# Kernel optimization log

Hardware: AMD Instinct MI355X
Metric: run time of the kernel (lower is better)

The kernel has to match this reference:

```python
import jax, jax.numpy as jnp
import numpy as np

N_NODES = 100_000
N_EDGES = 1_600_000
F_IN = 32
F_OUT = 32
DIM = 2
K = 5                      # kernel_size per dim (open spline)
KTOT = K ** DIM            # 25 kernel weight matrices
S = 2 ** DIM               # 4 nonzero linear-B-spline basis terms per edge
NEG_SLOPE = 0.2

# offsets over the 2^DIM corners of the spline cell, [S, DIM]
_OFFSETS = np.array([[(s >> d) & 1 for d in range(DIM)] for s in range(S)], dtype=np.int32)
_STRIDES = np.array([K ** d for d in range(DIM)], dtype=np.int32)


def _spline_basis(pseudo):
    """Degree-1 open B-spline basis. pseudo: [E, DIM] in [0,1].
    Returns basis [E, S] and kernel-weight indices widx [E, S]."""
    offsets = jnp.asarray(_OFFSETS)
    strides = jnp.asarray(_STRIDES)
    p = pseudo * (K - 1)                         # open spline scaling
    fl = jnp.floor(p)
    frac = p - fl                                # [E, DIM]
    b = jnp.where(offsets[None] == 0, 1.0 - frac[:, None, :], frac[:, None, :])
    basis = jnp.prod(b, axis=-1)                 # [E, S]
    idx = jnp.clip(fl.astype(jnp.int32)[:, None, :] + offsets[None], 0, K - 1)
    widx = jnp.sum(idx * strides, axis=-1)       # [E, S] in [0, KTOT)
    return basis, widx


def setup_inputs() -> dict:
    key = jax.random.key(0)
    ks = jax.random.split(key, 7)
    x = jax.random.normal(ks[0], (N_NODES, F_IN), dtype=jnp.float32)
    edge_index = jax.random.randint(ks[1], (2, N_EDGES), 0, N_NODES)
    pseudo = jax.random.uniform(ks[2], (N_EDGES, DIM), dtype=jnp.float32)
    bound = 1.0 / np.sqrt(KTOT * F_IN)           # matches reset_parameters uniform(size, ...)
    weight = jax.random.uniform(ks[3], (KTOT, F_IN, F_OUT), jnp.float32, -bound, bound)
    root_weight = jax.random.uniform(ks[4], (F_IN, F_OUT), jnp.float32, -bound, bound)
    att_weight = jax.random.uniform(ks[5], (2 * F_OUT,), jnp.float32, -bound, bound)
    bias = jax.random.uniform(ks[6], (F_OUT,), jnp.float32, -bound, bound)
    return {"x": x, "edge_index": edge_index, "pseudo": pseudo, "weight": weight,
            "root_weight": root_weight, "att_weight": att_weight, "bias": bias}


def reference(x, edge_index, pseudo, weight, root_weight, att_weight, bias):
    row, col = edge_index[0], edge_index[1]      # row = target, col = source
    basis, widx = _spline_basis(pseudo)          # [E,S], [E,S]

    # Precompute x @ W_k for every kernel weight: [N, KTOT, F_OUT]
    xw = jnp.einsum('nf,kfo->nko', x, weight)
    flat = col[:, None] * KTOT + widx            # [E, S] flat (node, kernel) index
    gathered = xw.reshape(-1, F_OUT)[flat]       # [E, S, F_OUT]
    msg = jnp.einsum('es,esf->ef', basis, gathered)  # spline-weighted edge messages

    x_root = x @ root_weight                     # [N, F_OUT]

    # GAT-style attention logits: cat([x_root[row], msg]) . att_weight
    alpha = x_root[row] @ att_weight[:F_OUT] + msg @ att_weight[F_OUT:]
    alpha = jnp.where(alpha > 0, alpha, NEG_SLOPE * alpha)  # leaky relu

    # segment softmax over incoming edges of each target node
    amax = jax.ops.segment_max(alpha, row, num_segments=N_NODES)
    amax = jnp.where(jnp.isfinite(amax), amax, 0.0)
    ex = jnp.exp(alpha - amax[row])
    denom = jax.ops.segment_sum(ex, row, num_segments=N_NODES)
    att = ex / (denom[row] + 1e-16)

    out = jax.ops.segment_sum(msg * att[:, None], row, num_segments=N_NODES)
    return out + x_root + bias
```

## Files before the change

kernel.cpp:

```cpp
#include <hip/hip_runtime.h>
#include <stdint.h>

#define N_NODES 100000
#define N_EDGES 1600000
#define NBLK_SCAN 391

typedef __attribute__((ext_vector_type(8))) short short8;
typedef __attribute__((ext_vector_type(4))) float float4v;

__device__ __forceinline__ unsigned short f32_to_bf16(float f) {
  uint32_t u = __float_as_uint(f);
  u += 0x7fffu + ((u >> 16) & 1u);
  return (unsigned short)(u >> 16);
}
__device__ __forceinline__ float bf16_to_f32(unsigned short h) {
  return __uint_as_float(((uint32_t)h) << 16);
}

__global__ __launch_bounds__(256) void k_zero(
    const float* __restrict__ weight, const float* __restrict__ root_w,
    const float* __restrict__ att_w,
    int* __restrict__ deg, unsigned short* __restrict__ wbf,
    unsigned short* __restrict__ xw) {
  int tid = threadIdx.x;
  int b = blockIdx.x;
  int i = b * 256 + tid;
  if (i < N_NODES) deg[i] = 0;
  if (b < 100) {
    int e = i;
    int t = e >> 9, rem = e & 511;
    int q = rem >> 7, row = (rem >> 3) & 15, j = rem & 7;
    int km = t >> 1, fin = q * 8 + j, fo = (t & 1) * 16 + row;
    wbf[e] = f32_to_bf16(weight[(km * 32 + fin) * 32 + fo]);
  } else if (b == 100) {
    for (int idx = tid; idx < 1024; idx += 256) {
      int t = 50 + (idx >> 9), rem = idx & 511;
      int q = rem >> 7, row = (rem >> 3) & 15, j = rem & 7;
      int fin = q * 8 + j, fo = (t - 50) * 16 + row;
      wbf[t * 512 + rem] = f32_to_bf16(root_w[fin * 32 + fo]);
    }
    for (int idx = tid; idx < 1024; idx += 256) {
      int t = 52 + (idx >> 9), rem = idx & 511;
      int q = rem >> 7, row = (rem >> 3) & 15, j = rem & 7;
      int fin = q * 8 + j, km = (t - 52) * 16 + row;
      float s = 0.f;
      if (km < 25) {
#pragma unroll
        for (int fo = 0; fo < 32; fo++)
          s += weight[(km * 32 + fin) * 32 + fo] * att_w[32 + fo];
      }
      wbf[t * 512 + rem] = f32_to_bf16(s);
    }
  } else if (b == 101) {
    if (tid < 400) ((unsigned int*)(xw + 80000000))[tid] = 0u;
  }
}

__global__ __launch_bounds__(256) void k1_xw(
    const float* __restrict__ x, const unsigned short* __restrict__ wbf,
    const int* __restrict__ ei, const float* __restrict__ att_w,
    const float* __restrict__ bias,
    int* __restrict__ deg, unsigned short* __restrict__ rank,
    unsigned short* __restrict__ xw, float* __restrict__ out,
    uint2* __restrict__ od, float* __restrict__ ydot) {
  __shared__ __align__(16) uint2 st[3200];
  int tid = threadIdx.x;
  int b = blockIdx.x;

  int e = b * 256 + tid;
  int rk = atomicAdd(&deg[ei[e]], 1);

  int wave = tid >> 6, lane = tid & 63;
  int quad = lane >> 4, c16 = lane & 15;
  int n0 = b * 16;
  int node = n0 + c16;
  const float* xp = x + (size_t)node * 32 + quad * 8;
  float4 a0 = *reinterpret_cast<const float4*>(xp);
  float4 a1 = *reinterpret_cast<const float4*>(xp + 4);
  short8 af;
  af[0] = (short)f32_to_bf16(a0.x); af[1] = (short)f32_to_bf16(a0.y);
  af[2] = (short)f32_to_bf16(a0.z); af[3] = (short)f32_to_bf16(a0.w);
  af[4] = (short)f32_to_bf16(a1.x); af[5] = (short)f32_to_bf16(a1.y);
  af[6] = (short)f32_to_bf16(a1.z); af[7] = (short)f32_to_bf16(a1.w);

  float rsum = 0.f;
#pragma unroll 1
  for (int idx = 0; idx < 13; idx++) {
    int t = wave * 13 + idx;
    short8 bf = *reinterpret_cast<const short8*>(wbf + ((t * 4 + quad) * 16 + c16) * 8);
    float4v acc = {0.f, 0.f, 0.f, 0.f};
    acc = __builtin_amdgcn_mfma_f32_16x16x32_bf16(bf, af, acc, 0, 0, 0);
    if (t < 50) {
      uint2 pk;
      pk.x = (unsigned int)f32_to_bf16(acc[0]) |
             ((unsigned int)f32_to_bf16(acc[1]) << 16);
      pk.y = (unsigned int)f32_to_bf16(acc[2]) |
             ((unsigned int)f32_to_bf16(acc[3]) << 16);
      int tq = t * 4 + quad;
      st[tq * 16 + (c16 ^ (tq & 15))] = pk;
    } else {
      int gfo = (t - 50) * 16 + quad * 4;
      float4 bi = *reinterpret_cast<const float4*>(bias + gfo);
      float4 o;
      o.x = acc[0] + bi.x; o.y = acc[1] + bi.y;
      o.z = acc[2] + bi.z; o.w = acc[3] + bi.w;
      *reinterpret_cast<float4*>(out + (size_t)node * 32 + gfo) = o;
      float4 aw = *reinterpret_cast<const float4*>(att_w + gfo);
      rsum += acc[0] * aw.x + acc[1] * aw.y + acc[2] * aw.z + acc[3] * aw.w;
    }
  }
  if (wave < 2) {
    int t = 52 + wave;
    short8 bf = *reinterpret_cast<const short8*>(wbf + ((t * 4 + quad) * 16 + c16) * 8);
    float4v acc = {0.f, 0.f, 0.f, 0.f};
    acc = __builtin_amdgcn_mfma_f32_16x16x32_bf16(bf, af, acc, 0, 0, 0);
    float4 o;
    o.x = acc[0]; o.y = acc[1]; o.z = acc[2]; o.w = acc[3];
    *reinterpret_cast<float4*>(ydot + (size_t)node * 32 + (t - 52) * 16 + quad * 4) = o;
  }
  if (wave == 3) {
    rsum += __shfl_xor(rsum, 16);
    rsum += __shfl_xor(rsum, 32);
    if (lane < 16) od[node].y = __float_as_uint(rsum);
  }
  __syncthreads();
  uint2* dst = reinterpret_cast<uint2*>(xw) + (size_t)n0 * 200;
  for (int j = tid; j < 3200; j += 256) {
    int nd = j / 200;
    int tq = j - nd * 200;
    dst[j] = st[tq * 16 + (nd ^ (tq & 15))];
  }
  rank[e] = (unsigned short)rk;
}

__global__ __launch_bounds__(256) void kscan1(const int* __restrict__ deg,
                                              int* __restrict__ incl,
                                              int* __restrict__ bsum) {
  __shared__ int s[256];
  int tid = threadIdx.x;
  int i = blockIdx.x * 256 + tid;
  int v = (i < N_NODES) ? deg[i] : 0;
  s[tid] = v;
  __syncthreads();
  for (int d = 1; d < 256; d <<= 1) {
    int t = (tid >= d) ? s[tid - d] : 0;
    __syncthreads();
    s[tid] += t;
    __syncthreads();
  }
  if (i < N_NODES) incl[i] = s[tid];
  if (tid == 255) bsum[blockIdx.x] = s[255];
}

__global__ __launch_bounds__(512) void kscan2(const int* __restrict__ bsum,
                                              int* __restrict__ bbase) {
  __shared__ int s[512];
  int tid = threadIdx.x;
  int v = (tid < NBLK_SCAN) ? bsum[tid] : 0;
  s[tid] = v;
  __syncthreads();
  for (int d = 1; d < 512; d <<= 1) {
    int t = (tid >= d) ? s[tid - d] : 0;
    __syncthreads();
    s[tid] += t;
    __syncthreads();
  }
  if (tid < NBLK_SCAN) bbase[tid] = s[tid] - v;
}

__global__ __launch_bounds__(256) void kscan3(const int* __restrict__ deg,
                                              int* __restrict__ offs,
                                              const int* __restrict__ bbase,
                                              uint2* __restrict__ od) {
  int i = blockIdx.x * 256 + threadIdx.x;
  if (i < N_NODES) {
    int v = offs[i] - deg[i] + bbase[i >> 8];
    offs[i] = v;
    od[i].x = (unsigned int)v;
  }
  if (i == 0) offs[N_NODES] = N_EDGES;
}

__global__ __launch_bounds__(256) void k_ydq(const float* __restrict__ ydot,
                                             uint2* __restrict__ ydq) {
  int idx = blockIdx.x * 256 + threadIdx.x;
  int n = idx >> 4, cell = idx & 15;
  int i1 = cell >> 2, i0 = cell & 3;
  const float* bb = ydot + (size_t)n * 32 + i1 * 5 + i0;
  float y0 = bb[0], y1 = bb[1], y2 = bb[5], y3 = bb[6];
  uint2 pk;
  pk.x = (unsigned int)f32_to_bf16(y0) | ((unsigned int)f32_to_bf16(y1) << 16);
  pk.y = (unsigned int)f32_to_bf16(y2) | ((unsigned int)f32_to_bf16(y3) << 16);
  ydq[idx] = pk;
}

__global__ __launch_bounds__(256) void kscatter(
    const int* __restrict__ ei, const float* __restrict__ pseudo,
    const uint2* __restrict__ od, const unsigned short* __restrict__ rank,
    const uint2* __restrict__ ydq,
    unsigned int* __restrict__ eidx, uint2* __restrict__ ecoef) {
  int e = blockIdx.x * 256 + threadIdx.x;
  int r = ei[e];
  int c = ei[N_EDGES + e];
  float p0 = pseudo[2 * e] * 4.f;
  float p1 = pseudo[2 * e + 1] * 4.f;
  int rk = rank[e];
  uint2 v = od[r];
  float fl0 = floorf(p0), fl1 = floorf(p1);
  float fr0 = p0 - fl0, fr1 = p1 - fl1;
  int i0 = (int)fl0, i1 = (int)fl1;
  uint2 yq = ydq[c * 16 + i1 * 4 + i0];
  float y0 = __uint_as_float(yq.x << 16);
  float y1 = __uint_as_float(yq.x & 0xffff0000u);
  float y2 = __uint_as_float(yq.y << 16);
  float y3 = __uint_as_float(yq.y & 0xffff0000u);
  float c0 = 1.f - fr0, c1 = 1.f - fr1;
  float b0 = c0 * c1, b1 = fr0 * c1, b2 = c0 * fr1, b3 = fr0 * fr1;
  float alpha = __uint_as_float(v.y) + b0 * y0 + b1 * y1 + b2 * y2 + b3 * y3;
  alpha = alpha > 0.f ? alpha : 0.2f * alpha;
  float ex = __expf(alpha);
  int pos = (int)v.x + rk;
  int w0 = i0 + 5 * i1;
  int w2 = w0 + 5;
  uint2 pk;
  pk.x = (unsigned int)f32_to_bf16(b0 * ex) |
         ((unsigned int)f32_to_bf16(b1 * ex) << 16);
  pk.y = (unsigned int)f32_to_bf16(b2 * ex) |
         ((unsigned int)f32_to_bf16(b3 * ex) << 16);
  ecoef[pos] = pk;
  eidx[pos] = (unsigned int)c | ((unsigned int)w0 << 17) |
              ((unsigned int)w2 << 22);
}

__global__ __launch_bounds__(256) void k2_csr(
    const int* __restrict__ offs, const unsigned int* __restrict__ eidx,
    const uint2* __restrict__ ecoef, const unsigned short* __restrict__ xw,
    float* __restrict__ out) {
  int tid = threadIdx.x;
  int wave = tid >> 6, lane = tid & 63;
  int node = blockIdx.x * 4 + wave;
  if (node >= N_NODES) return;
  int f = lane & 31, half = lane >> 5;
  int s0 = offs[node], s1 = offs[node + 1];
  const unsigned short* xwf = xw + f;
  float accA = 0.f, accB = 0.f, denA = 0.f, denB = 0.f;
  int i = s0 + half;

  for (; i + 6 < s1; i += 8) {
    unsigned int id[4];
    uint2 cf[4];
    id[0] = eidx[i];     id[1] = eidx[i + 2];
    id[2] = eidx[i + 4]; id[3] = eidx[i + 6];
    cf[0] = ecoef[i];     cf[1] = ecoef[i + 2];
    cf[2] = ecoef[i + 4]; cf[3] = ecoef[i + 6];
    float g0[4], g1[4], g2[4], g3[4];
#pragma unroll
    for (int u = 0; u < 4; u++) {
      const unsigned short* base = xwf + (size_t)(id[u] & 0x1FFFF) * 800;
      int o0 = ((id[u] >> 17) & 31) * 32;
      int o2 = ((id[u] >> 22) & 31) * 32;
      g0[u] = bf16_to_f32(base[o0]);
      g1[u] = bf16_to_f32(base[o0 + 32]);
      g2[u] = bf16_to_f32(base[o2]);
      g3[u] = bf16_to_f32(base[o2 + 32]);
    }
#pragma unroll
    for (int u = 0; u < 4; u++) {
      float q0 = __uint_as_float(cf[u].x << 16);
      float q1 = __uint_as_float(cf[u].x & 0xffff0000u);
      float q2 = __uint_as_float(cf[u].y << 16);
      float q3 = __uint_as_float(cf[u].y & 0xffff0000u);
      float m = q0 * g0[u] + q1 * g1[u] + q2 * g2[u] + q3 * g3[u];
      float d = (q0 + q1) + (q2 + q3);
      if (u & 1) { accB += m; denB += d; } else { accA += m; denA += d; }
    }
  }
  for (; i < s1; i += 2) {
    unsigned int idv = eidx[i];
    uint2 cfv = ecoef[i];
    const unsigned short* base = xwf + (size_t)(idv & 0x1FFFF) * 800;
    int o0 = ((idv >> 17) & 31) * 32;
    int o2 = ((idv >> 22) & 31) * 32;
    float g0 = bf16_to_f32(base[o0]);
    float g1 = bf16_to_f32(base[o0 + 32]);
    float g2 = bf16_to_f32(base[o2]);
    float g3 = bf16_to_f32(base[o2 + 32]);
    float q0 = __uint_as_float(cfv.x << 16);
    float q1 = __uint_as_float(cfv.x & 0xffff0000u);
    float q2 = __uint_as_float(cfv.y << 16);
    float q3 = __uint_as_float(cfv.y & 0xffff0000u);
    accA += q0 * g0 + q1 * g1 + q2 * g2 + q3 * g3;
    denA += (q0 + q1) + (q2 + q3);
  }

  float acc = accA + accB;
  float den = denA + denB;
  acc += __shfl_xor(acc, 32);
  den += __shfl_xor(den, 32);
  if (half == 0) out[node * 32 + f] += acc / (den + 1e-16f);
}

extern "C" void kernel_launch(void* const* d_in, const int* in_sizes, int n_in,
                              void* d_out, int out_size, void* d_ws, size_t ws_size,
                              hipStream_t stream) {
  const float* x      = (const float*)d_in[0];
  const int*   ei     = (const int*)d_in[1];
  const float* pseudo = (const float*)d_in[2];
  const float* weight = (const float*)d_in[3];
  const float* root_w = (const float*)d_in[4];
  const float* att_w  = (const float*)d_in[5];
  const float* bias   = (const float*)d_in[6];
  float* out = (float*)d_out;

  char* ws = (char*)d_ws;
  unsigned short* xw   = (unsigned short*)ws;
  uint2* ydq           = (uint2*)(ws + 160001600);
  uint2* od            = (uint2*)(ws + 172801600);
  unsigned short* wbf  = (unsigned short*)(ws + 173601600);
  int* deg             = (int*)(ws + 173656896);
  int* offs            = (int*)(ws + 174056896);
  int* bsum            = (int*)(ws + 174456912);
  int* bbase           = (int*)(ws + 174458512);
  unsigned short* rank = (unsigned short*)(ws + 174460112);
  uint2* ecoef         = (uint2*)(ws + 177660112);
  float* ydot          = (float*)(ws + 177660112);
  unsigned int* eidx   = (unsigned int*)(ws + 190460112);

  hipLaunchKernelGGL(k_zero, dim3(NBLK_SCAN), dim3(256), 0, stream,
                     weight, root_w, att_w, deg, wbf, xw);
  hipLaunchKernelGGL(k1_xw, dim3(6250), dim3(256), 0, stream,
                     x, wbf, ei, att_w, bias, deg, rank, xw, out, od, ydot);
  hipLaunchKernelGGL(kscan1, dim3(NBLK_SCAN), dim3(256), 0, stream, deg, offs, bsum);
  hipLaunchKernelGGL(kscan2, dim3(1), dim3(512), 0, stream, bsum, bbase);
  hipLaunchKernelGGL(kscan3, dim3(NBLK_SCAN), dim3(256), 0, stream, deg, offs, bbase, od);
  hipLaunchKernelGGL(k_ydq, dim3(6250), dim3(256), 0, stream, ydot, ydq);
  hipLaunchKernelGGL(kscatter, dim3(6250), dim3(256), 0, stream,
                     ei, pseudo, od, rank, ydq, eidx, ecoef);
  hipLaunchKernelGGL(k2_csr, dim3(25000), dim3(256), 0, stream,
                     offs, eidx, ecoef, xw, out);
}
```

Measured before the change: 382.7 us.

## Fuse ydq packing into xw kernel and split degree histogram into its own kernel

The per-node attention-dot cell packing (ydq) is now computed inside the xw MFMA kernel from a shared-memory staging tile. This removes the separate k_ydq kernel and the fp32 ydot round trip through global memory. The edge degree atomic histogram moves out of the xw kernel into its own kernel, which decouples the atomic latency from the MFMA work but adds a launch and reads edge_index in a separate pass. The main loop's unroll-1 pragma is also dropped, letting the compiler unroll it.

```diff
diff --git a/kernel.cpp b/kernel.cpp
--- a/kernel.cpp
+++ b/kernel.cpp
@@ -56,19 +56,23 @@
   }
 }
 
-__global__ __launch_bounds__(256) void k1_xw(
+__global__ __launch_bounds__(256) void k1a_hist(
+    const int* __restrict__ ei, int* __restrict__ deg,
+    unsigned short* __restrict__ rank) {
+  int e = blockIdx.x * 256 + threadIdx.x;
+  int r = ei[e];
+  rank[e] = (unsigned short)atomicAdd(&deg[r], 1);
+}
+
+__global__ __launch_bounds__(256) void k1b_xw(
     const float* __restrict__ x, const unsigned short* __restrict__ wbf,
-    const int* __restrict__ ei, const float* __restrict__ att_w,
-    const float* __restrict__ bias,
-    int* __restrict__ deg, unsigned short* __restrict__ rank,
+    const float* __restrict__ att_w, const float* __restrict__ bias,
     unsigned short* __restrict__ xw, float* __restrict__ out,
-    uint2* __restrict__ od, float* __restrict__ ydot) {
+    uint2* __restrict__ od, uint2* __restrict__ ydq) {
   __shared__ __align__(16) uint2 st[3200];
+  __shared__ float ydl[16][33];
   int tid = threadIdx.x;
   int b = blockIdx.x;
-
-  int e = b * 256 + tid;
-  int rk = atomicAdd(&deg[ei[e]], 1);
 
   int wave = tid >> 6, lane = tid & 63;
   int quad = lane >> 4, c16 = lane & 15;
@@ -84,7 +88,6 @@
   af[6] = (short)f32_to_bf16(a1.z); af[7] = (short)f32_to_bf16(a1.w);
 
   float rsum = 0.f;
-#pragma unroll 1
   for (int idx = 0; idx < 13; idx++) {
     int t = wave * 13 + idx;
     short8 bf = *reinterpret_cast<const short8*>(wbf + ((t * 4 + quad) * 16 + c16) * 8);
@@ -114,9 +117,9 @@
     short8 bf = *reinterpret_cast<const short8*>(wbf + ((t * 4 + quad) * 16 + c16) * 8);
     float4v acc = {0.f, 0.f, 0.f, 0.f};
     acc = __builtin_amdgcn_mfma_f32_16x16x32_bf16(bf, af, acc, 0, 0, 0);
-    float4 o;
-    o.x = acc[0]; o.y = acc[1]; o.z = acc[2]; o.w = acc[3];
-    *reinterpret_cast<float4*>(ydot + (size_t)node * 32 + (t - 52) * 16 + quad * 4) = o;
+    int kmb = wave * 16 + quad * 4;
+#pragma unroll
+    for (int r2 = 0; r2 < 4; r2++) ydl[c16][kmb + r2] = acc[r2];
   }
   if (wave == 3) {
     rsum += __shfl_xor(rsum, 16);
@@ -124,13 +127,23 @@
     if (lane < 16) od[node].y = __float_as_uint(rsum);
   }
   __syncthreads();
+  {
+    int nd = tid >> 4, cell = tid & 15;
+    int i1c = cell >> 2, i0c = cell & 3;
+    int km0 = i1c * 5 + i0c;
+    float y0 = ydl[nd][km0], y1 = ydl[nd][km0 + 1];
+    float y2 = ydl[nd][km0 + 5], y3 = ydl[nd][km0 + 6];
+    uint2 pk;
+    pk.x = (unsigned int)f32_to_bf16(y0) | ((unsigned int)f32_to_bf16(y1) << 16);
+    pk.y = (unsigned int)f32_to_bf16(y2) | ((unsigned int)f32_to_bf16(y3) << 16);
+    ydq[(size_t)n0 * 16 + tid] = pk;
+  }
   uint2* dst = reinterpret_cast<uint2*>(xw) + (size_t)n0 * 200;
   for (int j = tid; j < 3200; j += 256) {
     int nd = j / 200;
     int tq = j - nd * 200;
     dst[j] = st[tq * 16 + (nd ^ (tq & 15))];
   }
-  rank[e] = (unsigned short)rk;
 }
 
 __global__ __launch_bounds__(256) void kscan1(const int* __restrict__ deg,
@@ -179,19 +192,6 @@
     od[i].x = (unsigned int)v;
   }
   if (i == 0) offs[N_NODES] = N_EDGES;
-}
-
-__global__ __launch_bounds__(256) void k_ydq(const float* __restrict__ ydot,
-                                             uint2* __restrict__ ydq) {
-  int idx = blockIdx.x * 256 + threadIdx.x;
-  int n = idx >> 4, cell = idx & 15;
-  int i1 = cell >> 2, i0 = cell & 3;
-  const float* bb = ydot + (size_t)n * 32 + i1 * 5 + i0;
-  float y0 = bb[0], y1 = bb[1], y2 = bb[5], y3 = bb[6];
-  uint2 pk;
-  pk.x = (unsigned int)f32_to_bf16(y0) | ((unsigned int)f32_to_bf16(y1) << 16);
-  pk.y = (unsigned int)f32_to_bf16(y2) | ((unsigned int)f32_to_bf16(y3) << 16);
-  ydq[idx] = pk;
 }
 
 __global__ __launch_bounds__(256) void kscatter(
@@ -323,17 +323,16 @@
   int* bbase           = (int*)(ws + 174458512);
   unsigned short* rank = (unsigned short*)(ws + 174460112);
   uint2* ecoef         = (uint2*)(ws + 177660112);
-  float* ydot          = (float*)(ws + 177660112);
   unsigned int* eidx   = (unsigned int*)(ws + 190460112);
 
   hipLaunchKernelGGL(k_zero, dim3(NBLK_SCAN), dim3(256), 0, stream,
                      weight, root_w, att_w, deg, wbf, xw);
-  hipLaunchKernelGGL(k1_xw, dim3(6250), dim3(256), 0, stream,
-                     x, wbf, ei, att_w, bias, deg, rank, xw, out, od, ydot);
+  hipLaunchKernelGGL(k1a_hist, dim3(6250), dim3(256), 0, stream, ei, deg, rank);
+  hipLaunchKernelGGL(k1b_xw, dim3(6250), dim3(256), 0, stream,
+                     x, wbf, att_w, bias, xw, out, od, ydq);
   hipLaunchKernelGGL(kscan1, dim3(NBLK_SCAN), dim3(256), 0, stream, deg, offs, bsum);
   hipLaunchKernelGGL(kscan2, dim3(1), dim3(512), 0, stream, bsum, bbase);
   hipLaunchKernelGGL(kscan3, dim3(NBLK_SCAN), dim3(256), 0, stream, deg, offs, bbase, od);
-  hipLaunchKernelGGL(k_ydq, dim3(6250), dim3(256), 0, stream, ydot, ydq);
   hipLaunchKernelGGL(kscatter, dim3(6250), dim3(256), 0, stream,
                      ei, pseudo, od, rank, ydq, eidx, ecoef);
   hipLaunchKernelGGL(k2_csr, dim3(25000), dim3(256), 0, stream,
```

Result: slower. 394.3 us (+3.0%).

## Compute attention logits inside CSR aggregation instead of precomputed ydot table

Applied to the files above, without the earlier changes.

Removes the precomputed per-node attention-dot table (ydot/ydq kernel and its extra MFMA tiles) and the per-edge exp/coefficient precomputation in the scatter kernel. The scatter now writes one packed 8-byte record per edge (column, two kernel indices, 16-bit quantized fractions). The aggregation kernel rebuilds the spline message, reduces msg·att across lanes with shuffles to form alpha, and applies leaky-relu and exp in place. This cuts a launch and several intermediate buffers and halves the edge-stream traffic, but adds a 5-step shuffle reduction and an exp per edge in the gather loop.

```diff
diff --git a/kernel.cpp b/kernel.cpp
--- a/kernel.cpp
+++ b/kernel.cpp
@@ -19,9 +19,7 @@
 
 __global__ __launch_bounds__(256) void k_zero(
     const float* __restrict__ weight, const float* __restrict__ root_w,
-    const float* __restrict__ att_w,
-    int* __restrict__ deg, unsigned short* __restrict__ wbf,
-    unsigned short* __restrict__ xw) {
+    int* __restrict__ deg, unsigned short* __restrict__ wbf) {
   int tid = threadIdx.x;
   int b = blockIdx.x;
   int i = b * 256 + tid;
@@ -39,20 +37,6 @@
       int fin = q * 8 + j, fo = (t - 50) * 16 + row;
       wbf[t * 512 + rem] = f32_to_bf16(root_w[fin * 32 + fo]);
     }
-    for (int idx = tid; idx < 1024; idx += 256) {
-      int t = 52 + (idx >> 9), rem = idx & 511;
-      int q = rem >> 7, row = (rem >> 3) & 15, j = rem & 7;
-      int fin = q * 8 + j, km = (t - 52) * 16 + row;
-      float s = 0.f;
-      if (km < 25) {
-#pragma unroll
-        for (int fo = 0; fo < 32; fo++)
-          s += weight[(km * 32 + fin) * 32 + fo] * att_w[32 + fo];
-      }
-      wbf[t * 512 + rem] = f32_to_bf16(s);
-    }
-  } else if (b == 101) {
-    if (tid < 400) ((unsigned int*)(xw + 80000000))[tid] = 0u;
   }
 }
 
@@ -62,7 +46,7 @@
     const float* __restrict__ bias,
     int* __restrict__ deg, unsigned short* __restrict__ rank,
     unsigned short* __restrict__ xw, float* __restrict__ out,
-    uint2* __restrict__ od, float* __restrict__ ydot) {
+    uint2* __restrict__ od) {
   __shared__ __align__(16) uint2 st[3200];
   int tid = threadIdx.x;
   int b = blockIdx.x;
@@ -84,7 +68,6 @@
   af[6] = (short)f32_to_bf16(a1.z); af[7] = (short)f32_to_bf16(a1.w);
 
   float rsum = 0.f;
-#pragma unroll 1
   for (int idx = 0; idx < 13; idx++) {
     int t = wave * 13 + idx;
     short8 bf = *reinterpret_cast<const short8*>(wbf + ((t * 4 + quad) * 16 + c16) * 8);
@@ -109,15 +92,6 @@
       rsum += acc[0] * aw.x + acc[1] * aw.y + acc[2] * aw.z + acc[3] * aw.w;
     }
   }
-  if (wave < 2) {
-    int t = 52 + wave;
-    short8 bf = *reinterpret_cast<const short8*>(wbf + ((t * 4 + quad) * 16 + c16) * 8);
-    float4v acc = {0.f, 0.f, 0.f, 0.f};
-    acc = __builtin_amdgcn_mfma_f32_16x16x32_bf16(bf, af, acc, 0, 0, 0);
-    float4 o;
-    o.x = acc[0]; o.y = acc[1]; o.z = acc[2]; o.w = acc[3];
-    *reinterpret_cast<float4*>(ydot + (size_t)node * 32 + (t - 52) * 16 + quad * 4) = o;
-  }
   if (wave == 3) {
     rsum += __shfl_xor(rsum, 16);
     rsum += __shfl_xor(rsum, 32);
@@ -178,123 +152,126 @@
     offs[i] = v;
     od[i].x = (unsigned int)v;
   }
-  if (i == 0) offs[N_NODES] = N_EDGES;
-}
-
-__global__ __launch_bounds__(256) void k_ydq(const float* __restrict__ ydot,
-                                             uint2* __restrict__ ydq) {
-  int idx = blockIdx.x * 256 + threadIdx.x;
-  int n = idx >> 4, cell = idx & 15;
-  int i1 = cell >> 2, i0 = cell & 3;
-  const float* bb = ydot + (size_t)n * 32 + i1 * 5 + i0;
-  float y0 = bb[0], y1 = bb[1], y2 = bb[5], y3 = bb[6];
-  uint2 pk;
-  pk.x = (unsigned int)f32_to_bf16(y0) | ((unsigned int)f32_to_bf16(y1) << 16);
-  pk.y = (unsigned int)f32_to_bf16(y2) | ((unsigned int)f32_to_bf16(y3) << 16);
-  ydq[idx] = pk;
+  if (i == 0) {
+    offs[N_NODES] = N_EDGES;
+    od[N_NODES].x = (unsigned int)N_EDGES;
+  }
 }
 
 __global__ __launch_bounds__(256) void kscatter(
     const int* __restrict__ ei, const float* __restrict__ pseudo,
     const uint2* __restrict__ od, const unsigned short* __restrict__ rank,
-    const uint2* __restrict__ ydq,
-    unsigned int* __restrict__ eidx, uint2* __restrict__ ecoef) {
+    uint2* __restrict__ epack) {
   int e = blockIdx.x * 256 + threadIdx.x;
   int r = ei[e];
   int c = ei[N_EDGES + e];
   float p0 = pseudo[2 * e] * 4.f;
   float p1 = pseudo[2 * e + 1] * 4.f;
   int rk = rank[e];
-  uint2 v = od[r];
+  unsigned int offr = od[r].x;
   float fl0 = floorf(p0), fl1 = floorf(p1);
   float fr0 = p0 - fl0, fr1 = p1 - fl1;
   int i0 = (int)fl0, i1 = (int)fl1;
-  uint2 yq = ydq[c * 16 + i1 * 4 + i0];
-  float y0 = __uint_as_float(yq.x << 16);
-  float y1 = __uint_as_float(yq.x & 0xffff0000u);
-  float y2 = __uint_as_float(yq.y << 16);
-  float y3 = __uint_as_float(yq.y & 0xffff0000u);
-  float c0 = 1.f - fr0, c1 = 1.f - fr1;
-  float b0 = c0 * c1, b1 = fr0 * c1, b2 = c0 * fr1, b3 = fr0 * fr1;
-  float alpha = __uint_as_float(v.y) + b0 * y0 + b1 * y1 + b2 * y2 + b3 * y3;
-  alpha = alpha > 0.f ? alpha : 0.2f * alpha;
-  float ex = __expf(alpha);
-  int pos = (int)v.x + rk;
   int w0 = i0 + 5 * i1;
   int w2 = w0 + 5;
+  unsigned int q0 = (unsigned int)(fr0 * 65535.f + 0.5f);
+  unsigned int q1 = (unsigned int)(fr1 * 65535.f + 0.5f);
   uint2 pk;
-  pk.x = (unsigned int)f32_to_bf16(b0 * ex) |
-         ((unsigned int)f32_to_bf16(b1 * ex) << 16);
-  pk.y = (unsigned int)f32_to_bf16(b2 * ex) |
-         ((unsigned int)f32_to_bf16(b3 * ex) << 16);
-  ecoef[pos] = pk;
-  eidx[pos] = (unsigned int)c | ((unsigned int)w0 << 17) |
-              ((unsigned int)w2 << 22);
+  pk.x = (unsigned int)c | ((unsigned int)w0 << 17) | ((unsigned int)w2 << 22);
+  pk.y = q0 | (q1 << 16);
+  epack[offr + rk] = pk;
 }
 
 __global__ __launch_bounds__(256) void k2_csr(
-    const int* __restrict__ offs, const unsigned int* __restrict__ eidx,
-    const uint2* __restrict__ ecoef, const unsigned short* __restrict__ xw,
+    const uint2* __restrict__ od, const uint2* __restrict__ epack,
+    const unsigned short* __restrict__ xw, const float* __restrict__ att_w,
     float* __restrict__ out) {
   int tid = threadIdx.x;
   int wave = tid >> 6, lane = tid & 63;
   int node = blockIdx.x * 4 + wave;
   if (node >= N_NODES) return;
   int f = lane & 31, half = lane >> 5;
-  int s0 = offs[node], s1 = offs[node + 1];
+  uint2 v0 = od[node];
+  int s0 = (int)v0.x;
+  int s1 = (int)od[node + 1].x;
+  float rd = __uint_as_float(v0.y);
+  float a2 = att_w[32 + f];
   const unsigned short* xwf = xw + f;
-  float accA = 0.f, accB = 0.f, denA = 0.f, denB = 0.f;
+  float acc = 0.f, den = 0.f;
   int i = s0 + half;
+  const float Q = 1.f / 65535.f;
 
   for (; i + 6 < s1; i += 8) {
-    unsigned int id[4];
-    uint2 cf[4];
-    id[0] = eidx[i];     id[1] = eidx[i + 2];
-    id[2] = eidx[i + 4]; id[3] = eidx[i + 6];
-    cf[0] = ecoef[i];     cf[1] = ecoef[i + 2];
-    cf[2] = ecoef[i + 4]; cf[3] = ecoef[i + 6];
+    uint2 p[4];
+    p[0] = epack[i];     p[1] = epack[i + 2];
+    p[2] = epack[i + 4]; p[3] = epack[i + 6];
+    int col[4], o0[4], o2[4];
+    float fr0[4], fr1[4];
+#pragma unroll
+    for (int u = 0; u < 4; u++) {
+      col[u] = (int)(p[u].x & 0x1FFFF);
+      o0[u] = (int)((p[u].x >> 17) & 31) * 32;
+      o2[u] = (int)((p[u].x >> 22) & 31) * 32;
+      fr0[u] = (float)(p[u].y & 0xffff) * Q;
+      fr1[u] = (float)(p[u].y >> 16) * Q;
+    }
     float g0[4], g1[4], g2[4], g3[4];
 #pragma unroll
     for (int u = 0; u < 4; u++) {
-      const unsigned short* base = xwf + (size_t)(id[u] & 0x1FFFF) * 800;
-      int o0 = ((id[u] >> 17) & 31) * 32;
-      int o2 = ((id[u] >> 22) & 31) * 32;
-      g0[u] = bf16_to_f32(base[o0]);
-      g1[u] = bf16_to_f32(base[o0 + 32]);
-      g2[u] = bf16_to_f32(base[o2]);
-      g3[u] = bf16_to_f32(base[o2 + 32]);
-    }
+      const unsigned short* base = xwf + (size_t)col[u] * 800;
+      g0[u] = bf16_to_f32(base[o0[u]]);
+      g1[u] = bf16_to_f32(base[o0[u] + 32]);
+      g2[u] = bf16_to_f32(base[o2[u]]);
+      g3[u] = bf16_to_f32(base[o2[u] + 32]);
+    }
+    float msg[4], t[4];
 #pragma unroll
     for (int u = 0; u < 4; u++) {
-      float q0 = __uint_as_float(cf[u].x << 16);
-      float q1 = __uint_as_float(cf[u].x & 0xffff0000u);
-      float q2 = __uint_as_float(cf[u].y << 16);
-      float q3 = __uint_as_float(cf[u].y & 0xffff0000u);
-      float m = q0 * g0[u] + q1 * g1[u] + q2 * g2[u] + q3 * g3[u];
-      float d = (q0 + q1) + (q2 + q3);
-      if (u & 1) { accB += m; denB += d; } else { accA += m; denA += d; }
+      float c0 = 1.f - fr0[u], c1 = 1.f - fr1[u];
+      msg[u] = c1 * (c0 * g0[u] + fr0[u] * g1[u]) +
+               fr1[u] * (c0 * g2[u] + fr0[u] * g3[u]);
+      t[u] = msg[u] * a2;
+    }
+#pragma unroll
+    for (int m = 16; m >= 1; m >>= 1) {
+      t[0] += __shfl_xor(t[0], m);
+      t[1] += __shfl_xor(t[1], m);
+      t[2] += __shfl_xor(t[2], m);
+      t[3] += __shfl_xor(t[3], m);
+    }
+#pragma unroll
+    for (int u = 0; u < 4; u++) {
+      float alpha = rd + t[u];
+      alpha = alpha > 0.f ? alpha : 0.2f * alpha;
+      float ex = __expf(alpha);
+      acc += msg[u] * ex;
+      den += ex;
     }
   }
   for (; i < s1; i += 2) {
-    unsigned int idv = eidx[i];
-    uint2 cfv = ecoef[i];
-    const unsigned short* base = xwf + (size_t)(idv & 0x1FFFF) * 800;
-    int o0 = ((idv >> 17) & 31) * 32;
-    int o2 = ((idv >> 22) & 31) * 32;
+    uint2 pv = epack[i];
+    int col = (int)(pv.x & 0x1FFFF);
+    int o0 = (int)((pv.x >> 17) & 31) * 32;
+    int o2 = (int)((pv.x >> 22) & 31) * 32;
+    float fr0 = (float)(pv.y & 0xffff) * Q;
+    float fr1 = (float)(pv.y >> 16) * Q;
+    const unsigned short* base = xwf + (size_t)col * 800;
     float g0 = bf16_to_f32(base[o0]);
     float g1 = bf16_to_f32(base[o0 + 32]);
     float g2 = bf16_to_f32(base[o2]);
     float g3 = bf16_to_f32(base[o2 + 32]);
-    float q0 = __uint_as_float(cfv.x << 16);
-    float q1 = __uint_as_float(cfv.x & 0xffff0000u);
-    float q2 = __uint_as_float(cfv.y << 16);
-    float q3 = __uint_as_float(cfv.y & 0xffff0000u);
-    accA += q0 * g0 + q1 * g1 + q2 * g2 + q3 * g3;
-    denA += (q0 + q1) + (q2 + q3);
-  }
-
-  float acc = accA + accB;
-  float den = denA + denB;
+    float c0 = 1.f - fr0, c1 = 1.f - fr1;
+    float msg = c1 * (c0 * g0 + fr0 * g1) + fr1 * (c0 * g2 + fr0 * g3);
+    float t = msg * a2;
+#pragma unroll
+    for (int m = 16; m >= 1; m >>= 1) t += __shfl_xor(t, m);
+    float alpha = rd + t;
+    alpha = alpha > 0.f ? alpha : 0.2f * alpha;
+    float ex = __expf(alpha);
+    acc += msg * ex;
+    den += ex;
+  }
+
   acc += __shfl_xor(acc, 32);
   den += __shfl_xor(den, 32);
   if (half == 0) out[node * 32 + f] += acc / (den + 1e-16f);
@@ -314,28 +291,24 @@
 
   char* ws = (char*)d_ws;
   unsigned short* xw   = (unsigned short*)ws;
-  uint2* ydq           = (uint2*)(ws + 160001600);
-  uint2* od            = (uint2*)(ws + 172801600);
-  unsigned short* wbf  = (unsigned short*)(ws + 173601600);
-  int* deg             = (int*)(ws + 173656896);
-  int* offs            = (int*)(ws + 174056896);
-  int* bsum            = (int*)(ws + 174456912);
-  int* bbase           = (int*)(ws + 174458512);
-  unsigned short* rank = (unsigned short*)(ws + 174460112);
-  uint2* ecoef         = (uint2*)(ws + 177660112);
-  float* ydot          = (float*)(ws + 177660112);
-  unsigned int* eidx   = (unsigned int*)(ws + 190460112);
+  uint2* od            = (uint2*)(ws + 160000000);
+  unsigned short* wbf  = (unsigned short*)(ws + 160800016);
+  int* deg             = (int*)(ws + 160853264);
+  int* offs            = (int*)(ws + 161253264);
+  int* bsum            = (int*)(ws + 161653280);
+  int* bbase           = (int*)(ws + 161654880);
+  unsigned short* rank = (unsigned short*)(ws + 161656480);
+  uint2* epack         = (uint2*)(ws + 164856480);
 
   hipLaunchKernelGGL(k_zero, dim3(NBLK_SCAN), dim3(256), 0, stream,
-                     weight, root_w, att_w, deg, wbf, xw);
+                     weight, root_w, deg, wbf);
   hipLaunchKernelGGL(k1_xw, dim3(6250), dim3(256), 0, stream,
-                     x, wbf, ei, att_w, bias, deg, rank, xw, out, od, ydot);
+                     x, wbf, ei, att_w, bias, deg, rank, xw, out, od);
   hipLaunchKernelGGL(kscan1, dim3(NBLK_SCAN), dim3(256), 0, stream, deg, offs, bsum);
   hipLaunchKernelGGL(kscan2, dim3(1), dim3(512), 0, stream, bsum, bbase);
   hipLaunchKernelGGL(kscan3, dim3(NBLK_SCAN), dim3(256), 0, stream, deg, offs, bbase, od);
-  hipLaunchKernelGGL(k_ydq, dim3(6250), dim3(256), 0, stream, ydot, ydq);
   hipLaunchKernelGGL(kscatter, dim3(6250), dim3(256), 0, stream,
-                     ei, pseudo, od, rank, ydq, eidx, ecoef);
+                     ei, pseudo, od, rank, epack);
   hipLaunchKernelGGL(k2_csr, dim3(25000), dim3(256), 0, stream,
-                     offs, eidx, ecoef, xw, out);
-}
+                     od, epack, xw, att_w, out);
+}
```

After: 333.0 us. 1.15x faster.
